# Kernel tuning notes

Hardware: AMD Instinct MI355X
Metric: run time of the kernel (lower is better)

The kernel has to match this reference:

```python
import jax, jax.numpy as jnp
import numpy as np

FDIM = 128
NHEADS = 4
HDIM = FDIM // NHEADS
SIGMA2 = 2.0 * 0.3 ** 2


def _layernorm(h, w, b):
    m = h.mean(-1, keepdims=True)
    v = ((h - m) ** 2).mean(-1, keepdims=True)
    return (h - m) / jnp.sqrt(v + 1e-5) * w + b


def setup_inputs() -> dict:
    key = jax.random.key(0)
    ks = jax.random.split(key, 10)
    B, C, H, W = 16, FDIM, 128, 128
    Hm, Wm = 1024, 1024
    inp = {
        'x': jax.random.normal(ks[0], (B, C, H, W), jnp.float32),
        'masks': jax.random.uniform(ks[1], (B, 2, Hm, Wm), jnp.float32),
        'Wq': jax.random.normal(ks[2], (FDIM, FDIM), jnp.float32) * 0.02,
        'bq': jnp.zeros((FDIM,), jnp.float32),
        'Wk': jax.random.normal(ks[3], (FDIM, FDIM), jnp.float32) * 0.02,
        'bk': jnp.zeros((FDIM,), jnp.float32),
        'Wv': jax.random.normal(ks[4], (FDIM, FDIM), jnp.float32) * 0.02,
        'bv': jnp.zeros((FDIM,), jnp.float32),
        'Wo': jax.random.normal(ks[5], (FDIM, FDIM), jnp.float32) * 0.02,
        'bo': jnp.zeros((FDIM,), jnp.float32),
        'ln1_w': jnp.ones((FDIM,), jnp.float32),
        'ln1_b': jnp.zeros((FDIM,), jnp.float32),
        'W1': jax.random.normal(ks[6], (2 * FDIM, FDIM), jnp.float32) * 0.02,
        'b1': jnp.zeros((2 * FDIM,), jnp.float32),
        'W2': jax.random.normal(ks[7], (FDIM, 2 * FDIM), jnp.float32) * 0.02,
        'b2': jnp.zeros((FDIM,), jnp.float32),
        'ln2_w': jnp.ones((FDIM,), jnp.float32),
        'ln2_b': jnp.zeros((FDIM,), jnp.float32),
    }
    return inp


def reference(x, masks, Wq, bq, Wk, bk, Wv, bv, Wo, bo, ln1_w, ln1_b, W1, b1, W2, b2, ln2_w, ln2_b):
    B, C, H, W = x.shape
    Hm, Wm = masks.shape[2], masks.shape[3]
    # nearest-neighbor downsample of masks to feature-map size (torch 'nearest')
    iy = jnp.arange(H) * Hm // H
    ix = jnp.arange(W) * Wm // W
    m = masks[:, :, iy][:, :, :, ix]                      # (B, 2, H, W), raw values
    binm = (m > 0.5).astype(x.dtype)                       # thresholded for centroids

    # --- node pooling (vectorized extract_nodes_from_masks; both masks nonempty) ---
    nodes0 = jnp.einsum('bchw,bnhw->bnc', x, m) / (m.sum((2, 3))[..., None] + 1e-6)
    cnt = jnp.maximum(binm.sum((2, 3)), 1.0)               # (B, 2)
    ys = jnp.arange(H, dtype=x.dtype)
    xs = jnp.arange(W, dtype=x.dtype)
    cy = jnp.einsum('bnhw,h->bn', binm, ys) / cnt
    cx = jnp.einsum('bnhw,w->bn', binm, xs) / cnt
    pos = jnp.stack([cx / W * 2 - 1, cy / H * 2 - 1], -1)  # (B, N, 2) = (pos_x, pos_y)

    # --- distance-biased multi-head graph attention ---
    B_, N, _ = nodes0.shape
    def proj(t, Wp, bp):
        return (t @ Wp.T + bp).reshape(B_, N, NHEADS, HDIM).transpose(0, 2, 1, 3)
    Q = proj(nodes0, Wq, bq)
    K = proj(nodes0, Wk, bk)
    V = proj(nodes0, Wv, bv)
    scores = jnp.einsum('bhnd,bhmd->bhnm', Q, K) / (HDIM ** 0.5)
    d2 = jnp.sum((pos[:, :, None] - pos[:, None, :]) ** 2, -1)
    dist = jnp.where(d2 > 0, jnp.sqrt(jnp.where(d2 > 0, d2, 1.0)), 0.0)  # safe cdist
    attn = jax.nn.softmax(scores - dist[:, None], axis=-1)
    out = jnp.einsum('bhnm,bhmd->bhnd', attn, V).transpose(0, 2, 1, 3).reshape(B_, N, C)
    out = out @ Wo.T + bo
    nodes = _layernorm(nodes0 + out, ln1_w, ln1_b)
    ffn = jax.nn.relu(nodes @ W1.T + b1) @ W2.T + b2
    nodes = _layernorm(nodes + ffn, ln2_w, ln2_b)        # (B, N, C)

    # --- Gaussian broadcast of nodes back to the feature map ---
    yg = jnp.linspace(-1.0, 1.0, H)
    xg = jnp.linspace(-1.0, 1.0, W)
    dx = xg[None, None, None, :] - pos[:, :, 0][:, :, None, None]  # (B,N,1,W)
    dy = yg[None, None, :, None] - pos[:, :, 1][:, :, None, None]  # (B,N,H,1)
    wgt = jnp.exp(-(dx ** 2 + dy ** 2) / SIGMA2)                   # (B,N,H,W)
    graph_features = jnp.einsum('bnc,bnhw->bchw', nodes, wgt)
    return x + graph_features
```

## Files before the change

kernel.cpp:

```cpp
#include <hip/hip_runtime.h>
#include <cstdint>
#include <cstddef>

#define NB 16
#define NC 128
#define NH 128
#define NW 128
#define HM 1024
#define WM 1024
#define HW (NH*NW)
#define NHEADS 4
#define HDIM 32
#define INV_SIGMA2 5.555555555555555f

#define WS_M     0
#define WS_PART  524288
#define WS_NUM   525312
#define WS_NODES 529408
#define WS_WXY   533504

__global__ void kA(const float* __restrict__ masks, float* __restrict__ ws) {
    float* m_ds = ws + WS_M;
    float* part = ws + WS_PART;
    int blk = blockIdx.x;
    int b2 = blk >> 3;
    int chunk = blk & 7;
    int tid = threadIdx.x;
    int wcol = tid & 127;
    int rofs = tid >> 7;
    const float* mp = masks + (size_t)b2 * (HM * WM);
    float msum = 0.f, cnt = 0.f, cy = 0.f, cx = 0.f;
#pragma unroll
    for (int it = 0; it < 8; ++it) {
        int r = chunk * 16 + it * 2 + rofs;
        float v = mp[(size_t)(r * 8) * WM + wcol * 8];
        m_ds[(size_t)b2 * HW + r * 128 + wcol] = v;
        msum += v;
        if (v > 0.5f) { cnt += 1.0f; cy += (float)r; cx += (float)wcol; }
    }
    __shared__ float r0[256], r1[256], r2[256], r3[256];
    r0[tid] = msum; r1[tid] = cnt; r2[tid] = cy; r3[tid] = cx;
    __syncthreads();
    for (int s = 128; s > 0; s >>= 1) {
        if (tid < s) { r0[tid] += r0[tid+s]; r1[tid] += r1[tid+s];
                       r2[tid] += r2[tid+s]; r3[tid] += r3[tid+s]; }
        __syncthreads();
    }
    if (tid == 0) {
        float* p = part + (b2 * 8 + chunk) * 4;
        p[0] = r0[0]; p[1] = r1[0]; p[2] = r2[0]; p[3] = r3[0];
    }
}

__global__ void kB(const float* __restrict__ x, const float* __restrict__ ws_full) {
    const float* ws_m = ws_full + WS_M;
    float* num = (float*)(ws_full + WS_NUM);
    int b = blockIdx.x >> 7, c = blockIdx.x & 127;
    int tid = threadIdx.x;
    const float4* xp = (const float4*)(x + ((size_t)b * NC + c) * HW);
    const float4* m0 = (const float4*)(ws_m + (size_t)(b * 2 + 0) * HW);
    const float4* m1 = (const float4*)(ws_m + (size_t)(b * 2 + 1) * HW);
    float a0 = 0.f, a1 = 0.f;
#pragma unroll
    for (int i = 0; i < 16; ++i) {
        int idx = i * 256 + tid;
        float4 xv = xp[idx];
        float4 v0 = m0[idx];
        float4 v1 = m1[idx];
        a0 += xv.x*v0.x + xv.y*v0.y + xv.z*v0.z + xv.w*v0.w;
        a1 += xv.x*v1.x + xv.y*v1.y + xv.z*v1.z + xv.w*v1.w;
    }
    __shared__ float r0[256], r1[256];
    r0[tid] = a0; r1[tid] = a1;
    __syncthreads();
    for (int s = 128; s > 0; s >>= 1) {
        if (tid < s) { r0[tid] += r0[tid+s]; r1[tid] += r1[tid+s]; }
        __syncthreads();
    }
    if (tid == 0) {
        num[(b * 2 + 0) * 128 + c] = r0[0];
        num[(b * 2 + 1) * 128 + c] = r1[0];
    }
}

__device__ __forceinline__ float rowReduce(float v, float* red, int tid) {
    red[tid] = v;
    __syncthreads();
    int base = tid & 128;
    int lane = tid & 127;
    for (int s = 64; s > 0; s >>= 1) {
        if (lane < s) red[tid] += red[tid + s];
        __syncthreads();
    }
    float r = red[base];
    __syncthreads();
    return r;
}

__global__ void kC(const float* __restrict__ Wq, const float* __restrict__ bq,
                   const float* __restrict__ Wk, const float* __restrict__ bk,
                   const float* __restrict__ Wv, const float* __restrict__ bv,
                   const float* __restrict__ Wo, const float* __restrict__ bo,
                   const float* __restrict__ ln1w, const float* __restrict__ ln1b,
                   const float* __restrict__ W1, const float* __restrict__ b1,
                   const float* __restrict__ W2, const float* __restrict__ b2,
                   const float* __restrict__ ln2w, const float* __restrict__ ln2b,
                   float* __restrict__ ws) {
    int b = blockIdx.x;
    int tid = threadIdx.x;
    int c = tid & 127;
    int i = tid >> 7;

    const float* part = ws + WS_PART;
    const float* num  = ws + WS_NUM;
    float* nodesf = ws + WS_NODES;
    float* wxy    = ws + WS_WXY;

    __shared__ float s_n0[2][128], sQ[2][128], sK[2][128], sV[2][128];
    __shared__ float s_o[2][128], s_n1[2][128];
    __shared__ float s_hid[2][256];
    __shared__ float red[256];
    __shared__ float s_sc[16];
    __shared__ float s_at[NHEADS][2][2];
    __shared__ float s_px[2], s_py[2], s_den[2];

    if (tid < 2) {
        int n = tid;
        float msum = 0.f, cnt = 0.f, cy = 0.f, cx = 0.f;
        const float* p = part + ((b * 2 + n) * 8) * 4;
        for (int ch = 0; ch < 8; ++ch) {
            msum += p[ch*4+0]; cnt += p[ch*4+1]; cy += p[ch*4+2]; cx += p[ch*4+3];
        }
        s_den[n] = msum + 1e-6f;
        float cm = fmaxf(cnt, 1.0f);
        float cyv = cy / cm, cxv = cx / cm;
        s_px[n] = cxv / 64.0f - 1.0f;
        s_py[n] = cyv / 64.0f - 1.0f;
    }
    __syncthreads();

    s_n0[i][c] = num[(b * 2 + i) * 128 + c] / s_den[i];
    __syncthreads();

    {
        float aq = bq[c], ak = bk[c], av = bv[c];
        const float* wq = Wq + c * 128;
        const float* wk = Wk + c * 128;
        const float* wv = Wv + c * 128;
        for (int k = 0; k < 128; ++k) {
            float nv = s_n0[i][k];
            aq += nv * wq[k]; ak += nv * wk[k]; av += nv * wv[k];
        }
        sQ[i][c] = aq; sK[i][c] = ak; sV[i][c] = av;
    }
    __syncthreads();

    if (tid < 16) {
        int h = tid >> 2, ii = (tid >> 1) & 1, j = tid & 1;
        float s = 0.f;
        for (int d = 0; d < HDIM; ++d) s += sQ[ii][h*HDIM+d] * sK[j][h*HDIM+d];
        s *= 0.17677669529663687f;
        if (ii != j) {
            float dx = s_px[0] - s_px[1], dy = s_py[0] - s_py[1];
            float d2 = dx*dx + dy*dy;
            if (d2 > 0.f) s -= sqrtf(d2);
        }
        s_sc[tid] = s;
    }
    __syncthreads();

    if (tid < 8) {
        int h = tid >> 1, ii = tid & 1;
        float s0 = s_sc[h*4 + ii*2 + 0], s1 = s_sc[h*4 + ii*2 + 1];
        float mx = fmaxf(s0, s1);
        float e0 = expf(s0 - mx), e1 = expf(s1 - mx);
        float inv = 1.0f / (e0 + e1);
        s_at[h][ii][0] = e0 * inv;
        s_at[h][ii][1] = e1 * inv;
    }
    __syncthreads();

    {
        int h = c >> 5;
        s_o[i][c] = s_at[h][i][0] * sV[0][c] + s_at[h][i][1] * sV[1][c];
    }
    __syncthreads();

    float h1;
    {
        float acc = bo[c];
        const float* wo = Wo + c * 128;
        for (int k = 0; k < 128; ++k) acc += s_o[i][k] * wo[k];
        h1 = s_n0[i][c] + acc;
    }
    {
        float mean = rowReduce(h1, red, tid) * (1.0f / 128.0f);
        float d = h1 - mean;
        float var = rowReduce(d * d, red, tid) * (1.0f / 128.0f);
        float nrm = d * rsqrtf(var + 1e-5f);
        s_n1[i][c] = nrm * ln1w[c] + ln1b[c];
    }
    __syncthreads();

    for (int half = 0; half < 2; ++half) {
        int j = c + half * 128;
        float acc = b1[j];
        const float* w1 = W1 + j * 128;
        for (int k = 0; k < 128; ++k) acc += s_n1[i][k] * w1[k];
        s_hid[i][j] = fmaxf(acc, 0.0f);
    }
    __syncthreads();

    float h2;
    {
        float acc = b2[c];
        const float* w2 = W2 + c * 256;
        for (int j = 0; j < 256; ++j) acc += s_hid[i][j] * w2[j];
        h2 = s_n1[i][c] + acc;
    }
    {
        float mean = rowReduce(h2, red, tid) * (1.0f / 128.0f);
        float d = h2 - mean;
        float var = rowReduce(d * d, red, tid) * (1.0f / 128.0f);
        float nrm = d * rsqrtf(var + 1e-5f);
        nodesf[(b * 2 + i) * 128 + c] = nrm * ln2w[c] + ln2b[c];
    }
    {
        float g = (float)c * (2.0f / 127.0f) - 1.0f;
        float dx = g - s_px[i];
        float dy = g - s_py[i];
        wxy[((b*2+i)*2 + 0) * 128 + c] = expf(-dx * dx * INV_SIGMA2);
        wxy[((b*2+i)*2 + 1) * 128 + c] = expf(-dy * dy * INV_SIGMA2);
    }
}

__global__ void kD(const float* __restrict__ x, const float* __restrict__ ws,
                   float* __restrict__ out) {
    const float* nodesf = ws + WS_NODES;
    const float* wxy    = ws + WS_WXY;
    int b = blockIdx.x >> 7, c = blockIdx.x & 127;
    int tid = threadIdx.x;
    __shared__ float4 swx0[32], swx1[32];
    __shared__ float swy0[128], swy1[128];
    if (tid < 128) {
        swy0[tid] = wxy[((b*2+0)*2 + 1) * 128 + tid];
        swy1[tid] = wxy[((b*2+1)*2 + 1) * 128 + tid];
    } else {
        int t = tid - 128;
        if (t < 32)      swx0[t]      = ((const float4*)(wxy + ((b*2+0)*2 + 0) * 128))[t];
        else if (t < 64) swx1[t - 32] = ((const float4*)(wxy + ((b*2+1)*2 + 0) * 128))[t - 32];
    }
    float n0 = nodesf[(b * 2 + 0) * 128 + c];
    float n1 = nodesf[(b * 2 + 1) * 128 + c];
    __syncthreads();
    const float4* xp = (const float4*)(x   + ((size_t)b * NC + c) * HW);
    float4*       op = (float4*)      (out + ((size_t)b * NC + c) * HW);
#pragma unroll
    for (int it = 0; it < 16; ++it) {
        int p4 = it * 256 + tid;
        int h = p4 >> 5;
        int w4 = p4 & 31;
        float a0 = n0 * swy0[h];
        float a1 = n1 * swy1[h];
        float4 xv = xp[p4];
        float4 wx0 = swx0[w4], wx1 = swx1[w4];
        float4 r;
        r.x = xv.x + a0 * wx0.x + a1 * wx1.x;
        r.y = xv.y + a0 * wx0.y + a1 * wx1.y;
        r.z = xv.z + a0 * wx0.z + a1 * wx1.z;
        r.w = xv.w + a0 * wx0.w + a1 * wx1.w;
        op[p4] = r;
    }
}

extern "C" void kernel_launch(void* const* d_in, const int* in_sizes, int n_in,
                              void* d_out, int out_size, void* d_ws, size_t ws_size,
                              hipStream_t stream) {
    const float* x     = (const float*)d_in[0];
    const float* masks = (const float*)d_in[1];
    const float* Wq    = (const float*)d_in[2];
    const float* bq    = (const float*)d_in[3];
    const float* Wk    = (const float*)d_in[4];
    const float* bk    = (const float*)d_in[5];
    const float* Wv    = (const float*)d_in[6];
    const float* bv    = (const float*)d_in[7];
    const float* Wo    = (const float*)d_in[8];
    const float* bo    = (const float*)d_in[9];
    const float* ln1w  = (const float*)d_in[10];
    const float* ln1b  = (const float*)d_in[11];
    const float* W1    = (const float*)d_in[12];
    const float* b1    = (const float*)d_in[13];
    const float* W2    = (const float*)d_in[14];
    const float* b2    = (const float*)d_in[15];
    const float* ln2w  = (const float*)d_in[16];
    const float* ln2b  = (const float*)d_in[17];
    float* out = (float*)d_out;
    float* ws  = (float*)d_ws;

    hipLaunchKernelGGL(kA, dim3(NB * 2 * 8), dim3(256), 0, stream, masks, ws);
    hipLaunchKernelGGL(kB, dim3(NB * NC), dim3(256), 0, stream, x, ws);
    hipLaunchKernelGGL(kC, dim3(NB), dim3(256), 0, stream,
                       Wq, bq, Wk, bk, Wv, bv, Wo, bo, ln1w, ln1b,
                       W1, b1, W2, b2, ln2w, ln2b, ws);
    hipLaunchKernelGGL(kD, dim3(NB * NC), dim3(256), 0, stream, x, ws, out);
}
```

Before: 383.5 us.

## Use wavefront shuffle reductions and coalesced warp-cooperative GEMVs in node kernels

Replaces the shared-memory tree reductions in the mask-stat, pooling and layernorm steps with wavefront shuffle reductions plus a small cross-wave combine, which removes many barriers. It also rewrites the small per-batch matrix-vector products in the node transformer kernel. Instead of each thread reading a strided weight row, lanes now read coalesced float4 weight chunks and reduce across lanes with shuffles, handling both nodes together. Summation order changes slightly, and the dominant bandwidth-bound kernels are unchanged, so the effect on total time may be small.

```diff
diff --git a/kernel.cpp b/kernel.cpp
--- a/kernel.cpp
+++ b/kernel.cpp
@@ -18,6 +18,10 @@
 #define WS_NUM   525312
 #define WS_NODES 529408
 #define WS_WXY   533504
+
+__device__ __forceinline__ float dot4(float4 a, float4 b) {
+    return a.x*b.x + a.y*b.y + a.z*b.z + a.w*b.w;
+}
 
 __global__ void kA(const float* __restrict__ masks, float* __restrict__ ws) {
     float* m_ds = ws + WS_M;
@@ -38,17 +42,25 @@
         msum += v;
         if (v > 0.5f) { cnt += 1.0f; cy += (float)r; cx += (float)wcol; }
     }
-    __shared__ float r0[256], r1[256], r2[256], r3[256];
-    r0[tid] = msum; r1[tid] = cnt; r2[tid] = cy; r3[tid] = cx;
-    __syncthreads();
-    for (int s = 128; s > 0; s >>= 1) {
-        if (tid < s) { r0[tid] += r0[tid+s]; r1[tid] += r1[tid+s];
-                       r2[tid] += r2[tid+s]; r3[tid] += r3[tid+s]; }
-        __syncthreads();
-    }
+    __shared__ float wred[4][4];
+#pragma unroll
+    for (int s = 32; s > 0; s >>= 1) {
+        msum += __shfl_down(msum, s, 64);
+        cnt  += __shfl_down(cnt,  s, 64);
+        cy   += __shfl_down(cy,   s, 64);
+        cx   += __shfl_down(cx,   s, 64);
+    }
+    if ((tid & 63) == 0) {
+        int w = tid >> 6;
+        wred[w][0] = msum; wred[w][1] = cnt; wred[w][2] = cy; wred[w][3] = cx;
+    }
+    __syncthreads();
     if (tid == 0) {
         float* p = part + (b2 * 8 + chunk) * 4;
-        p[0] = r0[0]; p[1] = r1[0]; p[2] = r2[0]; p[3] = r3[0];
+        p[0] = wred[0][0] + wred[1][0] + wred[2][0] + wred[3][0];
+        p[1] = wred[0][1] + wred[1][1] + wred[2][1] + wred[3][1];
+        p[2] = wred[0][2] + wred[1][2] + wred[2][2] + wred[3][2];
+        p[3] = wred[0][3] + wred[1][3] + wred[2][3] + wred[3][3];
     }
 }
 
@@ -70,31 +82,18 @@
         a0 += xv.x*v0.x + xv.y*v0.y + xv.z*v0.z + xv.w*v0.w;
         a1 += xv.x*v1.x + xv.y*v1.y + xv.z*v1.z + xv.w*v1.w;
     }
-    __shared__ float r0[256], r1[256];
-    r0[tid] = a0; r1[tid] = a1;
-    __syncthreads();
-    for (int s = 128; s > 0; s >>= 1) {
-        if (tid < s) { r0[tid] += r0[tid+s]; r1[tid] += r1[tid+s]; }
-        __syncthreads();
-    }
+    __shared__ float wred[4][2];
+#pragma unroll
+    for (int s = 32; s > 0; s >>= 1) {
+        a0 += __shfl_down(a0, s, 64);
+        a1 += __shfl_down(a1, s, 64);
+    }
+    if ((tid & 63) == 0) { wred[tid >> 6][0] = a0; wred[tid >> 6][1] = a1; }
+    __syncthreads();
     if (tid == 0) {
-        num[(b * 2 + 0) * 128 + c] = r0[0];
-        num[(b * 2 + 1) * 128 + c] = r1[0];
-    }
-}
-
-__device__ __forceinline__ float rowReduce(float v, float* red, int tid) {
-    red[tid] = v;
-    __syncthreads();
-    int base = tid & 128;
-    int lane = tid & 127;
-    for (int s = 64; s > 0; s >>= 1) {
-        if (lane < s) red[tid] += red[tid + s];
-        __syncthreads();
-    }
-    float r = red[base];
-    __syncthreads();
-    return r;
+        num[(b * 2 + 0) * 128 + c] = wred[0][0] + wred[1][0] + wred[2][0] + wred[3][0];
+        num[(b * 2 + 1) * 128 + c] = wred[0][1] + wred[1][1] + wred[2][1] + wred[3][1];
+    }
 }
 
 __global__ void kC(const float* __restrict__ Wq, const float* __restrict__ bq,
@@ -116,10 +115,14 @@
     float* nodesf = ws + WS_NODES;
     float* wxy    = ws + WS_WXY;
 
-    __shared__ float s_n0[2][128], sQ[2][128], sK[2][128], sV[2][128];
-    __shared__ float s_o[2][128], s_n1[2][128];
-    __shared__ float s_hid[2][256];
-    __shared__ float red[256];
+    __shared__ __align__(16) float s_n0[2][128];
+    __shared__ __align__(16) float sQ[2][128], sK[2][128], sV[2][128];
+    __shared__ __align__(16) float s_o[2][128];
+    __shared__ __align__(16) float s_h1[2][128];
+    __shared__ __align__(16) float s_n1[2][128];
+    __shared__ __align__(16) float s_hid[2][256];
+    __shared__ __align__(16) float s_h2[2][128];
+    __shared__ float red[4];
     __shared__ float s_sc[16];
     __shared__ float s_at[NHEADS][2][2];
     __shared__ float s_px[2], s_py[2], s_den[2];
@@ -133,9 +136,8 @@
         }
         s_den[n] = msum + 1e-6f;
         float cm = fmaxf(cnt, 1.0f);
-        float cyv = cy / cm, cxv = cx / cm;
-        s_px[n] = cxv / 64.0f - 1.0f;
-        s_py[n] = cyv / 64.0f - 1.0f;
+        s_px[n] = (cx / cm) / 64.0f - 1.0f;
+        s_py[n] = (cy / cm) / 64.0f - 1.0f;
     }
     __syncthreads();
 
@@ -143,15 +145,32 @@
     __syncthreads();
 
     {
-        float aq = bq[c], ak = bk[c], av = bv[c];
-        const float* wq = Wq + c * 128;
-        const float* wk = Wk + c * 128;
-        const float* wv = Wv + c * 128;
-        for (int k = 0; k < 128; ++k) {
-            float nv = s_n0[i][k];
-            aq += nv * wq[k]; ak += nv * wk[k]; av += nv * wv[k];
-        }
-        sQ[i][c] = aq; sK[i][c] = ak; sV[i][c] = av;
+        float4 na0 = ((const float4*)s_n0[0])[tid & 31];
+        float4 na1 = ((const float4*)s_n0[1])[tid & 31];
+        const float4* Wq4 = (const float4*)Wq;
+        const float4* Wk4 = (const float4*)Wk;
+        const float4* Wv4 = (const float4*)Wv;
+#pragma unroll 4
+        for (int p = 0; p < 16; ++p) {
+            int e4 = p * 256 + tid;
+            float4 wq = Wq4[e4], wk = Wk4[e4], wv = Wv4[e4];
+            int cc = e4 >> 5;
+            float q0 = dot4(wq, na0), q1 = dot4(wq, na1);
+            float k0v = dot4(wk, na0), k1v = dot4(wk, na1);
+            float v0 = dot4(wv, na0), v1 = dot4(wv, na1);
+#pragma unroll
+            for (int s = 16; s > 0; s >>= 1) {
+                q0  += __shfl_down(q0,  s, 32); q1  += __shfl_down(q1,  s, 32);
+                k0v += __shfl_down(k0v, s, 32); k1v += __shfl_down(k1v, s, 32);
+                v0  += __shfl_down(v0,  s, 32); v1  += __shfl_down(v1,  s, 32);
+            }
+            if ((tid & 31) == 0) {
+                float bQ = bq[cc], bK = bk[cc], bV = bv[cc];
+                sQ[0][cc] = q0 + bQ;  sQ[1][cc] = q1 + bQ;
+                sK[0][cc] = k0v + bK; sK[1][cc] = k1v + bK;
+                sV[0][cc] = v0 + bV;  sV[1][cc] = v1 + bV;
+            }
+        }
     }
     __syncthreads();
 
@@ -186,45 +205,114 @@
     }
     __syncthreads();
 
-    float h1;
-    {
-        float acc = bo[c];
-        const float* wo = Wo + c * 128;
-        for (int k = 0; k < 128; ++k) acc += s_o[i][k] * wo[k];
-        h1 = s_n0[i][c] + acc;
-    }
-    {
-        float mean = rowReduce(h1, red, tid) * (1.0f / 128.0f);
-        float d = h1 - mean;
-        float var = rowReduce(d * d, red, tid) * (1.0f / 128.0f);
-        float nrm = d * rsqrtf(var + 1e-5f);
-        s_n1[i][c] = nrm * ln1w[c] + ln1b[c];
-    }
-    __syncthreads();
-
-    for (int half = 0; half < 2; ++half) {
-        int j = c + half * 128;
-        float acc = b1[j];
-        const float* w1 = W1 + j * 128;
-        for (int k = 0; k < 128; ++k) acc += s_n1[i][k] * w1[k];
-        s_hid[i][j] = fmaxf(acc, 0.0f);
-    }
-    __syncthreads();
-
-    float h2;
-    {
-        float acc = b2[c];
-        const float* w2 = W2 + c * 256;
-        for (int j = 0; j < 256; ++j) acc += s_hid[i][j] * w2[j];
-        h2 = s_n1[i][c] + acc;
-    }
-    {
-        float mean = rowReduce(h2, red, tid) * (1.0f / 128.0f);
-        float d = h2 - mean;
-        float var = rowReduce(d * d, red, tid) * (1.0f / 128.0f);
-        float nrm = d * rsqrtf(var + 1e-5f);
-        nodesf[(b * 2 + i) * 128 + c] = nrm * ln2w[c] + ln2b[c];
-    }
+    {
+        float4 oa0 = ((const float4*)s_o[0])[tid & 31];
+        float4 oa1 = ((const float4*)s_o[1])[tid & 31];
+        const float4* Wo4 = (const float4*)Wo;
+#pragma unroll 4
+        for (int p = 0; p < 16; ++p) {
+            int e4 = p * 256 + tid;
+            float4 w = Wo4[e4];
+            int cc = e4 >> 5;
+            float v0 = dot4(w, oa0), v1 = dot4(w, oa1);
+#pragma unroll
+            for (int s = 16; s > 0; s >>= 1) {
+                v0 += __shfl_down(v0, s, 32); v1 += __shfl_down(v1, s, 32);
+            }
+            if ((tid & 31) == 0) {
+                float bb = bo[cc];
+                s_h1[0][cc] = v0 + bb + s_n0[0][cc];
+                s_h1[1][cc] = v1 + bb + s_n0[1][cc];
+            }
+        }
+    }
+    __syncthreads();
+
+    {
+        float h = s_h1[i][c];
+        float v = h;
+#pragma unroll
+        for (int s = 32; s > 0; s >>= 1) v += __shfl_down(v, s, 64);
+        if ((tid & 63) == 0) red[tid >> 6] = v;
+        __syncthreads();
+        float mean = (red[i*2] + red[i*2+1]) * (1.0f / 128.0f);
+        float d = h - mean;
+        float v2 = d * d;
+        __syncthreads();
+#pragma unroll
+        for (int s = 32; s > 0; s >>= 1) v2 += __shfl_down(v2, s, 64);
+        if ((tid & 63) == 0) red[tid >> 6] = v2;
+        __syncthreads();
+        float var = (red[i*2] + red[i*2+1]) * (1.0f / 128.0f);
+        s_n1[i][c] = d * rsqrtf(var + 1e-5f) * ln1w[c] + ln1b[c];
+    }
+    __syncthreads();
+
+    {
+        float4 na0 = ((const float4*)s_n1[0])[tid & 31];
+        float4 na1 = ((const float4*)s_n1[1])[tid & 31];
+        const float4* W1_4 = (const float4*)W1;
+#pragma unroll 4
+        for (int p = 0; p < 32; ++p) {
+            int e4 = p * 256 + tid;
+            float4 w = W1_4[e4];
+            int j = e4 >> 5;
+            float v0 = dot4(w, na0), v1 = dot4(w, na1);
+#pragma unroll
+            for (int s = 16; s > 0; s >>= 1) {
+                v0 += __shfl_down(v0, s, 32); v1 += __shfl_down(v1, s, 32);
+            }
+            if ((tid & 31) == 0) {
+                float bb = b1[j];
+                s_hid[0][j] = fmaxf(v0 + bb, 0.0f);
+                s_hid[1][j] = fmaxf(v1 + bb, 0.0f);
+            }
+        }
+    }
+    __syncthreads();
+
+    {
+        float4 ha0 = ((const float4*)s_hid[0])[tid & 63];
+        float4 ha1 = ((const float4*)s_hid[1])[tid & 63];
+        const float4* W2_4 = (const float4*)W2;
+#pragma unroll 4
+        for (int p = 0; p < 32; ++p) {
+            int e4 = p * 256 + tid;
+            float4 w = W2_4[e4];
+            int cc = e4 >> 6;
+            float v0 = dot4(w, ha0), v1 = dot4(w, ha1);
+#pragma unroll
+            for (int s = 32; s > 0; s >>= 1) {
+                v0 += __shfl_down(v0, s, 64); v1 += __shfl_down(v1, s, 64);
+            }
+            if ((tid & 63) == 0) {
+                float bb = b2[cc];
+                s_h2[0][cc] = v0 + bb + s_n1[0][cc];
+                s_h2[1][cc] = v1 + bb + s_n1[1][cc];
+            }
+        }
+    }
+    __syncthreads();
+
+    {
+        float h = s_h2[i][c];
+        float v = h;
+#pragma unroll
+        for (int s = 32; s > 0; s >>= 1) v += __shfl_down(v, s, 64);
+        if ((tid & 63) == 0) red[tid >> 6] = v;
+        __syncthreads();
+        float mean = (red[i*2] + red[i*2+1]) * (1.0f / 128.0f);
+        float d = h - mean;
+        float v2 = d * d;
+        __syncthreads();
+#pragma unroll
+        for (int s = 32; s > 0; s >>= 1) v2 += __shfl_down(v2, s, 64);
+        if ((tid & 63) == 0) red[tid >> 6] = v2;
+        __syncthreads();
+        float var = (red[i*2] + red[i*2+1]) * (1.0f / 128.0f);
+        nodesf[(b * 2 + i) * 128 + c] = d * rsqrtf(var + 1e-5f) * ln2w[c] + ln2b[c];
+    }
+
     {
         float g = (float)c * (2.0f / 127.0f) - 1.0f;
         float dx = g - s_px[i];
```

Result: slower. 423.4 us (+10.4%).
